# Kernel tuning notes

Hardware: AMD Instinct MI355X
Metric: run time of the kernel (lower is better)

## Reference

```python
import jax, jax.numpy as jnp
import numpy as np

N, E, IN_FT, OUT_FT = 20000, 4096, 128, 128


def setup_inputs() -> dict:
    key = jax.random.key(0)
    kx, kh, kw = jax.random.split(key, 3)
    X = jax.random.normal(kx, (N, IN_FT), dtype=jnp.float32)
    H = jax.random.randint(kh, (N, E), 0, 2, dtype=jnp.int32)
    weight = jax.random.normal(kw, (IN_FT, OUT_FT), dtype=jnp.float32) * (1.0 / np.sqrt(IN_FT))
    bias = jnp.zeros((OUT_FT,), dtype=jnp.float32)
    return {"X": X, "H": H, "weight": weight, "bias": bias}


def reference(X, H, weight, bias):
    # Dv^{-1/2} H De^{-1} H^T Dv^{-1/2} X W + b, with diag matrices fused as
    # row/column scalings (same math as the torch.diag @ chain, no NxN temporaries).
    Hf = H.astype(jnp.float32)
    v_deg = jnp.sum(Hf, axis=1)            # [N]
    e_deg = jnp.sum(Hf, axis=0)            # [E]
    v_deg = jnp.where(v_deg > 0, v_deg, 1.0)
    e_deg = jnp.where(e_deg > 0, e_deg, 1.0)
    dv_inv_sqrt = 1.0 / jnp.sqrt(v_deg)    # diag(Dv^-1/2)
    de_inv = 1.0 / e_deg                   # diag(De^-1)
    Y = dv_inv_sqrt[:, None] * X
    T = Hf.T @ Y                           # H^T (...)        [E, in]
    T = de_inv[:, None] * T                # De^-1 (...)
    Z = Hf @ T                             # H (...)          [N, in]
    Z = dv_inv_sqrt[:, None] * Z           # Dv^-1/2 (...)
    out = Z @ weight + bias                # [N, out]
    return out
```

## Files before the change

kernel.cpp:

```cpp
#include <hip/hip_runtime.h>

#define NV 20000
#define NE 4096
#define FT 128
#define NW_E 128
#define NKC2 157
#define K_TOT 20096

typedef __attribute__((ext_vector_type(8))) short short8v;
typedef __attribute__((ext_vector_type(4))) float float4v;

__device__ __forceinline__ unsigned short f2bf(float f) {
    unsigned u = __float_as_uint(f);
    u += 0x7FFFu + ((u >> 16) & 1u);
    return (unsigned short)(u >> 16);
}
__device__ __forceinline__ int lds_off(int r, int c) {
    return r * 256 + ((c ^ (r & 15)) << 4);
}
__device__ __forceinline__ uint4 lut_entry(int t) {
    uint4 e;
    e.x = ((t & 1) ? 0x3F80u : 0u) | ((t & 2) ? 0x3F800000u : 0u);
    e.y = ((t & 4) ? 0x3F80u : 0u) | ((t & 8) ? 0x3F800000u : 0u);
    e.z = ((t & 16) ? 0x3F80u : 0u) | ((t & 32) ? 0x3F800000u : 0u);
    e.w = ((t & 64) ? 0x3F80u : 0u) | ((t & 128) ? 0x3F800000u : 0u);
    return e;
}
__device__ __forceinline__ void cp16(void* l, const void* g) {
    __builtin_amdgcn_global_load_lds((__attribute__((address_space(1))) void*)g,
                                     (__attribute__((address_space(3))) void*)l, 16, 0, 0);
}
__device__ __forceinline__ unsigned bt32(unsigned x, int lane) {
    unsigned y;
    y = __shfl_xor(x, 16, 64);
    x = (lane & 16) ? ((x & 0xFFFF0000u) | ((y >> 16) & 0x0000FFFFu))
                    : ((x & 0x0000FFFFu) | ((y << 16) & 0xFFFF0000u));
    y = __shfl_xor(x, 8, 64);
    x = (lane & 8)  ? ((x & 0xFF00FF00u) | ((y >> 8) & 0x00FF00FFu))
                    : ((x & 0x00FF00FFu) | ((y << 8) & 0xFF00FF00u));
    y = __shfl_xor(x, 4, 64);
    x = (lane & 4)  ? ((x & 0xF0F0F0F0u) | ((y >> 4) & 0x0F0F0F0Fu))
                    : ((x & 0x0F0F0F0Fu) | ((y << 4) & 0xF0F0F0F0u));
    y = __shfl_xor(x, 2, 64);
    x = (lane & 2)  ? ((x & 0xCCCCCCCCu) | ((y >> 2) & 0x33333333u))
                    : ((x & 0x33333333u) | ((y << 2) & 0xCCCCCCCCu));
    y = __shfl_xor(x, 1, 64);
    x = (lane & 1)  ? ((x & 0xAAAAAAAAu) | ((y >> 1) & 0x55555555u))
                    : ((x & 0x55555555u) | ((y << 1) & 0xAAAAAAAAu));
    return x;
}

__global__ __launch_bounds__(256) void k_pack(const int* __restrict__ H,
                                              unsigned* __restrict__ packed,
                                              float* __restrict__ dv,
                                              int* __restrict__ de_cnt) {
    __shared__ int cl[4];
    int t = threadIdx.x, wave = t >> 6, lane = t & 63;
    if (blockIdx.x < 16) de_cnt[blockIdx.x * 256 + t] = 0;
    int row = blockIdx.x * 2 + (wave >> 1);
    int half = wave & 1;
    const uint4* base = reinterpret_cast<const uint4*>(H) + (size_t)row * 1024 + half * 512 + lane * 8;
    unsigned m = 0;
#pragma unroll
    for (int i = 0; i < 8; ++i) {
        uint4 v = base[i];
        m |= (v.x ? 1u : 0u) << (i * 4 + 0);
        m |= (v.y ? 1u : 0u) << (i * 4 + 1);
        m |= (v.z ? 1u : 0u) << (i * 4 + 2);
        m |= (v.w ? 1u : 0u) << (i * 4 + 3);
    }
    packed[(size_t)row * NW_E + half * 64 + lane] = m;
    int c = __popc(m);
    for (int o = 32; o > 0; o >>= 1) c += __shfl_down(c, o, 64);
    if (lane == 0) cl[wave] = c;
    __syncthreads();
    if (t < 2) {
        int d = cl[t * 2] + cl[t * 2 + 1];
        dv[blockIdx.x * 2 + t] = d > 0 ? 1.0f / sqrtf((float)d) : 1.0f;
    }
}

__global__ __launch_bounds__(256) void k_mid(const float* __restrict__ X,
                                             const float* __restrict__ dv,
                                             unsigned short* __restrict__ At) {
    int t = threadIdx.x;
    int f = t & 127;
    int item = blockIdx.x * 2 + (t >> 7);
    int nbase = item * 8;
    unsigned short h[8];
#pragma unroll
    for (int i = 0; i < 8; ++i) {
        int n = nbase + i;
        float v = (n < NV) ? X[(size_t)n * FT + f] * dv[n] : 0.0f;
        h[i] = f2bf(v);
    }
    uint4 u;
    u.x = (unsigned)h[0] | ((unsigned)h[1] << 16);
    u.y = (unsigned)h[2] | ((unsigned)h[3] << 16);
    u.z = (unsigned)h[4] | ((unsigned)h[5] << 16);
    u.w = (unsigned)h[6] | ((unsigned)h[7] << 16);
    int kc2 = nbase >> 7;
    int c = (nbase >> 3) & 15;
    *reinterpret_cast<uint4*>(At + (size_t)kc2 * 16384 + f * 128 + ((c ^ (f & 15)) << 3)) = u;
}

__global__ __launch_bounds__(256, 2) void k_mm1(const unsigned short* __restrict__ At,
                                                const unsigned* __restrict__ packed,
                                                float* __restrict__ P,
                                                int* __restrict__ de_cnt, int chunkK) {
    __shared__ __align__(16) unsigned char sA[32768];
    __shared__ __align__(16) unsigned char sB[32768];
    __shared__ __align__(16) uint4 slut[256];
    int t = threadIdx.x;
    slut[t] = lut_entry(t);

    int et = blockIdx.x & 31, kp = blockIdx.x >> 5;
    int e0 = et * 128;
    int kbeg = kp * chunkK;
    int kend = kbeg + chunkK; if (kend > K_TOT) kend = K_TOT;
    int iters = (kend - kbeg) >> 7; if (iters < 0) iters = 0;

    float4v acc[4][4];
#pragma unroll
    for (int i = 0; i < 4; ++i)
#pragma unroll
        for (int j = 0; j < 4; ++j)
#pragma unroll
            for (int r = 0; r < 4; ++r) acc[i][j][r] = 0.0f;

    int wave = t >> 6, lane = t & 63;
    int wm0 = (wave & 1) * 64, wc0 = (wave >> 1) * 64;
    int r0 = lane & 15, q = lane >> 4;

    int grp = t >> 5, l32 = t & 31;
    int ns = grp & 3;
    int wbase = (grp >> 2) * 2;
    int ecol = et * 4 + wbase;
    int de_c0 = 0, de_c1 = 0;

    auto ldB = [&](int it) {
        uint2 v; v.x = 0u; v.y = 0u;
        int n = kbeg + it * 128 + ns * 32 + l32;
        if (n < NV) v = *reinterpret_cast<const uint2*>(packed + (size_t)n * NW_E + ecol);
        return v;
    };
    uint2 bw; bw.x = 0u; bw.y = 0u;
    if (iters > 0) bw = ldB(0);
    __syncthreads();

    const char* gA = reinterpret_cast<const char*>(At) + (size_t)(kbeg >> 7) * 32768 + wave * 8192 + lane * 16;
    char* lA = reinterpret_cast<char*>(sA) + wave * 8192;

    int rB0 = wbase * 32 + l32;
    int rB1 = rB0 + 32;

    for (int it = 0; it < iters; ++it) {
        const char* g = gA + (size_t)it * 32768;
#pragma unroll
        for (int j = 0; j < 8; ++j) cp16(lA + j * 1024, g + j * 1024);
        uint2 nxt; nxt.x = 0u; nxt.y = 0u;
        if (it + 1 < iters) nxt = ldB(it + 1);
        {
            unsigned x0 = bt32(bw.x, lane);
            unsigned x1 = bt32(bw.y, lane);
            de_c0 += __popc(x0);
            de_c1 += __popc(x1);
#pragma unroll
            for (int c = 0; c < 4; ++c)
                *reinterpret_cast<uint4*>(sB + lds_off(rB0, ns * 4 + c)) = slut[(x0 >> (c * 8)) & 0xFF];
#pragma unroll
            for (int c = 0; c < 4; ++c)
                *reinterpret_cast<uint4*>(sB + lds_off(rB1, ns * 4 + c)) = slut[(x1 >> (c * 8)) & 0xFF];
            bw = nxt;
        }
        __syncthreads();
#pragma unroll
        for (int ks = 0; ks < 4; ++ks) {
            short8v a[4], bb[4];
#pragma unroll
            for (int mi = 0; mi < 4; ++mi)
                a[mi] = *reinterpret_cast<const short8v*>(sA + lds_off(wm0 + mi * 16 + r0, ks * 4 + q));
#pragma unroll
            for (int ci = 0; ci < 4; ++ci)
                bb[ci] = *reinterpret_cast<const short8v*>(sB + lds_off(wc0 + ci * 16 + r0, ks * 4 + q));
#pragma unroll
            for (int mi = 0; mi < 4; ++mi)
#pragma unroll
                for (int ci = 0; ci < 4; ++ci)
                    acc[mi][ci] = __builtin_amdgcn_mfma_f32_16x16x32_bf16(a[mi], bb[ci], acc[mi][ci], 0, 0, 0);
        }
        __syncthreads();
    }
    atomicAdd(de_cnt + e0 + rB0, de_c0);
    atomicAdd(de_cnt + e0 + rB1, de_c1);
    float* Pp = P + (size_t)kp * (4096 * 128);
#pragma unroll
    for (int mi = 0; mi < 4; ++mi)
#pragma unroll
        for (int ci = 0; ci < 4; ++ci) {
            int f = wm0 + mi * 16 + q * 4;
            int e = e0 + wc0 + ci * 16 + r0;
            *reinterpret_cast<float4v*>(Pp + (size_t)e * 128 + f) = acc[mi][ci];
        }
}

__global__ __launch_bounds__(256) void k_redut(const float* __restrict__ P,
                                               const float* __restrict__ W,
                                               const int* __restrict__ de_cnt,
                                               unsigned short* __restrict__ Ut, int S) {
    __shared__ float sT[8][132];
    int t = threadIdx.x;
    int e0 = blockIdx.x * 8;
    {
        int el = t >> 5, fq = (t & 31) * 4;
        const float* base = P + (size_t)(e0 + el) * 128 + fq;
        float4 s = {0.f, 0.f, 0.f, 0.f};
        for (int p = 0; p < S; ++p) {
            float4 v = *reinterpret_cast<const float4*>(base + (size_t)p * 524288);
            s.x += v.x; s.y += v.y; s.z += v.z; s.w += v.w;
        }
        *reinterpret_cast<float4*>(&sT[el][fq]) = s;
    }
    __syncthreads();
    int el = t & 7, gq = (t >> 3) * 4;
    int e = e0 + el;
    float a0 = 0, a1 = 0, a2 = 0, a3 = 0;
    for (int f = 0; f < 128; ++f) {
        float tv = sT[el][f];
        float4 wv = *reinterpret_cast<const float4*>(W + f * 128 + gq);
        a0 += tv * wv.x; a1 += tv * wv.y; a2 += tv * wv.z; a3 += tv * wv.w;
    }
    int cnt = de_cnt[e];
    float d = cnt > 0 ? 1.0f / (float)cnt : 1.0f;
    float av[4] = {a0, a1, a2, a3};
    int slabB = e >> 7, chi = (e >> 3) & 15, pos = e & 7;
#pragma unroll
    for (int k = 0; k < 4; ++k) {
        int g = gq + k, qg = g >> 5, gr = g & 31;
        Ut[(size_t)(qg * 32 + slabB) * 4096 + gr * 128 + ((chi ^ (gr & 15)) << 3) + pos] = f2bf(av[k] * d);
    }
}

__global__ __launch_bounds__(256, 3) void k_mm2(const unsigned* __restrict__ packed,
                                                const unsigned short* __restrict__ Ut,
                                                const float* __restrict__ dv,
                                                const float* __restrict__ bias,
                                                float* __restrict__ out) {
    __shared__ __align__(16) unsigned char sA[32768];
    __shared__ __align__(16) unsigned char sB[8192];
    __shared__ __align__(16) uint4 slut[256];
    int t = threadIdx.x;
    slut[t] = lut_entry(t);

    int mt = blockIdx.x >> 2, qg = blockIdx.x & 3;
    int n0 = mt * 128, g0 = qg * 32;

    float4v acc[4];
#pragma unroll
    for (int i = 0; i < 4; ++i)
#pragma unroll
        for (int r = 0; r < 4; ++r) acc[i][r] = 0.0f;

    int wave = t >> 6, lane = t & 63;
    int wm0 = (wave & 1) * 64, wc0 = (wave >> 1) * 16;
    int r0 = lane & 15, q = lane >> 4;

    int rA = t & 127, half = t >> 7, cb = half << 3;
    const uint4* arow4 = reinterpret_cast<const uint4*>(packed + (size_t)(n0 + rA) * NW_E);
    uint4 aw = arow4[0];
    __syncthreads();

    const char* gB = reinterpret_cast<const char*>(Ut) + (size_t)(qg * 32) * 8192 + (wave & 1) * 4096 + lane * 16;
    char* lB = reinterpret_cast<char*>(sB) + (wave & 1) * 4096;

    for (int it = 0; it < 32; ++it) {
        uint4 nxt = arow4[it + 1];
        if (wave < 2) {
            const char* g = gB + (size_t)it * 8192;
#pragma unroll
            for (int j = 0; j < 4; ++j) cp16(lB + j * 1024, g + j * 1024);
        }
        {
            unsigned wd0 = half ? aw.z : aw.x;
            unsigned wd1 = half ? aw.w : aw.y;
#pragma unroll
            for (int c = 0; c < 4; ++c)
                *reinterpret_cast<uint4*>(sA + lds_off(rA, cb + c)) = slut[(wd0 >> (c * 8)) & 0xFF];
#pragma unroll
            for (int c = 0; c < 4; ++c)
                *reinterpret_cast<uint4*>(sA + lds_off(rA, cb + 4 + c)) = slut[(wd1 >> (c * 8)) & 0xFF];
            aw = nxt;
        }
        __syncthreads();
#pragma unroll
        for (int ks = 0; ks < 4; ++ks) {
            short8v a[4], bb;
#pragma unroll
            for (int mi = 0; mi < 4; ++mi)
                a[mi] = *reinterpret_cast<const short8v*>(sA + lds_off(wm0 + mi * 16 + r0, ks * 4 + q));
            bb = *reinterpret_cast<const short8v*>(sB + lds_off(wc0 + r0, ks * 4 + q));
#pragma unroll
            for (int mi = 0; mi < 4; ++mi)
                acc[mi] = __builtin_amdgcn_mfma_f32_16x16x32_bf16(a[mi], bb, acc[mi], 0, 0, 0);
        }
        __syncthreads();
    }
    {
        int g = g0 + wc0 + r0;
        float bg = bias[g];
#pragma unroll
        for (int mi = 0; mi < 4; ++mi) {
#pragma unroll
            for (int r = 0; r < 4; ++r) {
                int n = n0 + wm0 + mi * 16 + q * 4 + r;
                if (n < NV) out[(size_t)n * 128 + g] = dv[n] * acc[mi][r] + bg;
            }
        }
    }
}

extern "C" void kernel_launch(void* const* d_in, const int* in_sizes, int n_in,
                              void* d_out, int out_size, void* d_ws, size_t ws_size,
                              hipStream_t stream) {
    const float* X    = (const float*)d_in[0];
    const int*   H    = (const int*)d_in[1];
    const float* W    = (const float*)d_in[2];
    const float* bias = (const float*)d_in[3];
    float* out = (float*)d_out;

    char* ws = (char*)d_ws;
    size_t off = 0;
    auto alloc = [&](size_t sz) { char* p = ws + off; off += (sz + 255) & ~(size_t)255; return p; };
    unsigned*       packed  = (unsigned*)alloc((size_t)NV * NW_E * 4);
    unsigned short* At      = (unsigned short*)alloc((size_t)NKC2 * 16384 * 2);
    unsigned short* Ut      = (unsigned short*)alloc((size_t)FT * NE * 2);
    float*          dv      = (float*)alloc((size_t)NV * 4);
    int*            de_cnt  = (int*)alloc((size_t)NE * 4);
    size_t fixed = off;

    long long avail = (long long)ws_size - (long long)fixed;
    int S = (int)(avail / (128LL * 4096 * 4));
    if (S > 16) S = 16;
    if (S < 1) S = 1;
    float* P1 = (float*)(ws + fixed);
    int chunkK = ((NKC2 + S - 1) / S) * 128;

    k_pack  <<<NV / 2, 256, 0, stream>>>(H, packed, dv, de_cnt);
    k_mid   <<<1256, 256, 0, stream>>>(X, dv, At);
    k_mm1   <<<32 * S, 256, 0, stream>>>(At, packed, P1, de_cnt, chunkK);
    k_redut <<<512, 256, 0, stream>>>(P1, W, de_cnt, Ut, S);
    k_mm2   <<<628, 256, 0, stream>>>(packed, Ut, dv, bias, out);
}
```

Before: 559.4 us.

## Split k_mm2 over edge dimension with full-width output tiles and atomic accumulation

k_mm2 now gives each block a 128-row tile across all 128 output features and one quarter of the edge (K) range. Before, each block covered a 32-feature slice and looped over all edges. This means the packed incidence bits are expanded once per K slice and not repeated for each feature group, and each wave does 16 MFMAs per A load. Partial results are combined with float atomicAdd into the output, which k_redut now pre-fills with the bias. The cost is 4x atomic traffic on the output, a nondeterministic summation order, and a larger LDS and register footprint that lowers occupancy to 2 blocks per CU.

```diff
diff --git a/kernel.cpp b/kernel.cpp
--- a/kernel.cpp
+++ b/kernel.cpp
@@ -207,9 +207,17 @@
 __global__ __launch_bounds__(256) void k_redut(const float* __restrict__ P,
                                                const float* __restrict__ W,
                                                const int* __restrict__ de_cnt,
-                                               unsigned short* __restrict__ Ut, int S) {
+                                               unsigned short* __restrict__ Ut,
+                                               float* __restrict__ out,
+                                               const float* __restrict__ bias, int S) {
     __shared__ float sT[8][132];
     int t = threadIdx.x;
+    {
+        const float4* b4 = reinterpret_cast<const float4*>(bias);
+        float4* o4 = reinterpret_cast<float4*>(out);
+        for (int i = blockIdx.x * 256 + t; i < NV * 32; i += 512 * 256)
+            o4[i] = b4[i & 31];
+    }
     int e0 = blockIdx.x * 8;
     {
         int el = t >> 5, fq = (t & 31) * 4;
@@ -241,44 +249,45 @@
     }
 }
 
-__global__ __launch_bounds__(256, 3) void k_mm2(const unsigned* __restrict__ packed,
+__global__ __launch_bounds__(256, 2) void k_mm2(const unsigned* __restrict__ packed,
                                                 const unsigned short* __restrict__ Ut,
                                                 const float* __restrict__ dv,
-                                                const float* __restrict__ bias,
                                                 float* __restrict__ out) {
     __shared__ __align__(16) unsigned char sA[32768];
-    __shared__ __align__(16) unsigned char sB[8192];
+    __shared__ __align__(16) unsigned char sB[32768];
     __shared__ __align__(16) uint4 slut[256];
     int t = threadIdx.x;
     slut[t] = lut_entry(t);
 
-    int mt = blockIdx.x >> 2, qg = blockIdx.x & 3;
-    int n0 = mt * 128, g0 = qg * 32;
-
-    float4v acc[4];
+    int mt = blockIdx.x >> 2, es = blockIdx.x & 3;
+    int n0 = mt * 128;
+
+    float4v acc[4][4];
 #pragma unroll
     for (int i = 0; i < 4; ++i)
 #pragma unroll
-        for (int r = 0; r < 4; ++r) acc[i][r] = 0.0f;
+        for (int j = 0; j < 4; ++j)
+#pragma unroll
+            for (int r = 0; r < 4; ++r) acc[i][j][r] = 0.0f;
 
     int wave = t >> 6, lane = t & 63;
-    int wm0 = (wave & 1) * 64, wc0 = (wave >> 1) * 16;
+    int wm0 = (wave & 1) * 64, wg0 = (wave >> 1) * 64;
     int r0 = lane & 15, q = lane >> 4;
 
     int rA = t & 127, half = t >> 7, cb = half << 3;
-    const uint4* arow4 = reinterpret_cast<const uint4*>(packed + (size_t)(n0 + rA) * NW_E);
+    const uint4* arow4 = reinterpret_cast<const uint4*>(packed + (size_t)(n0 + rA) * NW_E) + es * 8;
     uint4 aw = arow4[0];
     __syncthreads();
 
-    const char* gB = reinterpret_cast<const char*>(Ut) + (size_t)(qg * 32) * 8192 + (wave & 1) * 4096 + lane * 16;
-    char* lB = reinterpret_cast<char*>(sB) + (wave & 1) * 4096;
-
-    for (int it = 0; it < 32; ++it) {
+    const char* gB = reinterpret_cast<const char*>(Ut) + ((size_t)wave * 32 + es * 8) * 8192 + lane * 16;
+    char* lB = reinterpret_cast<char*>(sB) + wave * 8192;
+
+    for (int it = 0; it < 8; ++it) {
         uint4 nxt = arow4[it + 1];
-        if (wave < 2) {
+        {
             const char* g = gB + (size_t)it * 8192;
 #pragma unroll
-            for (int j = 0; j < 4; ++j) cp16(lB + j * 1024, g + j * 1024);
+            for (int j = 0; j < 8; ++j) cp16(lB + j * 1024, g + j * 1024);
         }
         {
             unsigned wd0 = half ? aw.z : aw.x;
@@ -294,29 +303,32 @@
         __syncthreads();
 #pragma unroll
         for (int ks = 0; ks < 4; ++ks) {
-            short8v a[4], bb;
+            short8v a[4], bb[4];
 #pragma unroll
             for (int mi = 0; mi < 4; ++mi)
                 a[mi] = *reinterpret_cast<const short8v*>(sA + lds_off(wm0 + mi * 16 + r0, ks * 4 + q));
-            bb = *reinterpret_cast<const short8v*>(sB + lds_off(wc0 + r0, ks * 4 + q));
+#pragma unroll
+            for (int ci = 0; ci < 4; ++ci)
+                bb[ci] = *reinterpret_cast<const short8v*>(sB + lds_off(wg0 + ci * 16 + r0, ks * 4 + q));
 #pragma unroll
             for (int mi = 0; mi < 4; ++mi)
-                acc[mi] = __builtin_amdgcn_mfma_f32_16x16x32_bf16(a[mi], bb, acc[mi], 0, 0, 0);
+#pragma unroll
+                for (int ci = 0; ci < 4; ++ci)
+                    acc[mi][ci] = __builtin_amdgcn_mfma_f32_16x16x32_bf16(a[mi], bb[ci], acc[mi][ci], 0, 0, 0);
         }
         __syncthreads();
     }
-    {
-        int g = g0 + wc0 + r0;
-        float bg = bias[g];
-#pragma unroll
-        for (int mi = 0; mi < 4; ++mi) {
+#pragma unroll
+    for (int mi = 0; mi < 4; ++mi)
+#pragma unroll
+        for (int ci = 0; ci < 4; ++ci) {
+            int g = wg0 + ci * 16 + r0;
 #pragma unroll
             for (int r = 0; r < 4; ++r) {
                 int n = n0 + wm0 + mi * 16 + q * 4 + r;
-                if (n < NV) out[(size_t)n * 128 + g] = dv[n] * acc[mi][r] + bg;
+                if (n < NV) atomicAdd(out + (size_t)n * 128 + g, dv[n] * acc[mi][ci][r]);
             }
         }
-    }
 }
 
 extern "C" void kernel_launch(void* const* d_in, const int* in_sizes, int n_in,
@@ -348,6 +360,6 @@
     k_pack  <<<NV / 2, 256, 0, stream>>>(H, packed, dv, de_cnt);
     k_mid   <<<1256, 256, 0, stream>>>(X, dv, At);
     k_mm1   <<<32 * S, 256, 0, stream>>>(At, packed, P1, de_cnt, chunkK);
-    k_redut <<<512, 256, 0, stream>>>(P1, W, de_cnt, Ut, S);
-    k_mm2   <<<628, 256, 0, stream>>>(packed, Ut, dv, bias, out);
-}
+    k_redut <<<512, 256, 0, stream>>>(P1, W, de_cnt, Ut, out, bias, S);
+    k_mm2   <<<628, 256, 0, stream>>>(packed, Ut, dv, out);
+}
```

After: 570.3 us. About the same (+1.9%).
